# Kernel optimization log

Measured on AMD Instinct MI355X. Metric: run time of the kernel, lower is better.

Reference implementation:

```python
import jax, jax.numpy as jnp
import numpy as np

N_NODES = 50000
N_EDGES = 800000
NODE_DIM = 64
EDGE_DIM = 32
HIDDEN = 128
OUT_DIM = 32
N_LAYERS = 3
NUM_GRAPHS = 128


def setup_inputs() -> dict:
    key = jax.random.key(0)
    ks = jax.random.split(key, 20)
    s = 0.05
    inp = {
        "x": jax.random.normal(ks[0], (N_NODES, NODE_DIM), dtype=jnp.float32),
        "edge_attr": jax.random.normal(ks[1], (N_EDGES, EDGE_DIM), dtype=jnp.float32),
        "edge_index": jax.random.randint(ks[2], (2, N_EDGES), 0, N_NODES, dtype=jnp.int32),
        "batch": jnp.sort(jax.random.randint(ks[3], (N_NODES,), 0, NUM_GRAPHS, dtype=jnp.int32)),
        # per-interaction params, stacked on leading layer axis
        "W_dense": jax.random.normal(ks[4], (N_LAYERS, NODE_DIM, NODE_DIM)) * s,
        "filt_W1": jax.random.normal(ks[5], (N_LAYERS, EDGE_DIM, HIDDEN)) * s,
        "filt_b1": jnp.zeros((N_LAYERS, HIDDEN)),
        "filt_W2": jax.random.normal(ks[6], (N_LAYERS, HIDDEN, NODE_DIM)) * s,
        "filt_b2": jnp.zeros((N_LAYERS, NODE_DIM)),
        "attn_v": jax.random.normal(ks[7], (N_LAYERS, NODE_DIM)) * s,
        "out_W1": jax.random.normal(ks[8], (N_LAYERS, NODE_DIM, HIDDEN)) * s,
        "out_b1": jnp.zeros((N_LAYERS, HIDDEN)),
        "out_W2": jax.random.normal(ks[9], (N_LAYERS, HIDDEN, NODE_DIM)) * s,
        "out_b2": jnp.zeros((N_LAYERS, NODE_DIM)),
        # output network
        "net_W1": jax.random.normal(ks[10], (NODE_DIM, HIDDEN)) * s,
        "net_b1": jnp.zeros((HIDDEN,)),
        "net_W2": jax.random.normal(ks[11], (HIDDEN, OUT_DIM)) * s,
        "net_b2": jnp.zeros((OUT_DIM,)),
    }
    return inp


def _mlp2(x, W1, b1, W2, b2):
    # 2-layer MLP with tanh after first layer (matches MLP(num_layers=2, act='tanh'))
    return jnp.tanh(x @ W1 + b1) @ W2 + b2


def reference(x, edge_attr, W_dense, filt_W1, filt_b1, filt_W2, filt_b2,
              attn_v, out_W1, out_b1, out_W2, out_b2,
              net_W1, net_b1, net_W2, net_b2, edge_index, batch):
    n_nodes = x.shape[0]
    src, tgt = edge_index[0], edge_index[1]
    h = x
    for i in range(N_LAYERS):
        hd = h @ W_dense[i]                                   # initial_dense (no bias)
        edge_w = _mlp2(edge_attr, filt_W1[i], filt_b1[i], filt_W2[i], filt_b2[i])  # [E, D]
        messages = hd[src] * edge_w                           # [E, D]
        # per-target segment softmax over attention scores
        scores = messages @ attn_v[i]                         # [E]
        seg_max = jax.ops.segment_max(scores, tgt, num_segments=n_nodes)
        exp_s = jnp.exp(scores - seg_max[tgt])
        denom = jax.ops.segment_sum(exp_s, tgt, num_segments=n_nodes)
        attn_w = exp_s / denom[tgt]                           # [E]
        messages = messages * attn_w[:, None]
        agg = jax.ops.segment_sum(messages, tgt, num_segments=n_nodes)  # [N, D]
        delta = _mlp2(agg, out_W1[i], out_b1[i], out_W2[i], out_b2[i])
        h = h + delta                                         # residual
    # mean pooling per graph
    pooled = jax.ops.segment_sum(h, batch, num_segments=NUM_GRAPHS)
    counts = jnp.bincount(batch, length=NUM_GRAPHS)
    pooled = pooled / jnp.maximum(counts, 1)[:, None].astype(h.dtype)
    out = _mlp2(pooled, net_W1, net_b1, net_W2, net_b2)       # [G, OUT_DIM]
    return out
```

## Files before the change

### kernel.cpp

```cpp
#include <hip/hip_runtime.h>
#include <hip/hip_bf16.h>
#include <math.h>

#define NODE_DIM 64
#define EDGE_DIM 32
#define HIDDEN   128
#define OUT_DIM  32
#define N_LAYERS 3
#define NGRAPH   128

typedef __attribute__((ext_vector_type(8))) short bf16x8;
typedef __attribute__((ext_vector_type(4))) float f32x4;

__device__ __forceinline__ unsigned short f2bf(float f) {
    unsigned u = __float_as_uint(f);
    u = (u + 0x7fffu + ((u >> 16) & 1u)) >> 16;
    return (unsigned short)u;
}
__device__ __forceinline__ float bf2f(unsigned short h) {
    return __uint_as_float((unsigned)h << 16);
}
__device__ __forceinline__ float fast_tanh(float x) {
    float e = __expf(-2.f * x);
    float r = __builtin_amdgcn_rcpf(1.f + e);
    return __builtin_fmaf(2.f, r, -1.f);
}

__global__ __launch_bounds__(256) void coarse_hist_kernel(
    const int* __restrict__ tgt, int* __restrict__ Hc, int E, int C, int NB) {
    __shared__ int lh[512];
    int blk = blockIdx.x, tid = threadIdx.x;
    for (int b = tid; b < C; b += 256) lh[b] = 0;
    __syncthreads();
    int base = blk * 4096;
#pragma unroll
    for (int i = 0; i < 16; ++i) {
        int e = base + i * 256 + tid;
        if (e < E) atomicAdd(&lh[tgt[e] >> 7], 1);
    }
    __syncthreads();
    for (int b = tid; b < C; b += 256) Hc[(size_t)b * NB + blk] = lh[b];
}

__global__ __launch_bounds__(256) void scan1_kernel(const int* __restrict__ c,
                                                    int* __restrict__ o,
                                                    int* __restrict__ bsum, int n) {
    __shared__ int sh[256];
    int b = blockIdx.x, t = threadIdx.x;
    int i = b * 256 + t;
    int v = (i < n) ? c[i] : 0;
    sh[t] = v;
    __syncthreads();
    for (int d = 1; d < 256; d <<= 1) {
        int u = (t >= d) ? sh[t - d] : 0;
        __syncthreads();
        sh[t] += u;
        __syncthreads();
    }
    if (i < n) o[i] = sh[t] - v;
    if (t == 255) bsum[b] = sh[255];
}

__global__ void scan2_kernel(int* __restrict__ bsum, int nb) {
    __shared__ int sh[1024];
    int t = threadIdx.x;
    int v = (t < nb) ? bsum[t] : 0;
    sh[t] = v;
    __syncthreads();
    for (int d = 1; d < 1024; d <<= 1) {
        int u = (t >= d) ? sh[t - d] : 0;
        __syncthreads();
        sh[t] += u;
        __syncthreads();
    }
    if (t < nb) bsum[t] = sh[t] - v;
}

__global__ __launch_bounds__(256) void scan3_kernel(int* __restrict__ o,
                                                    const int* __restrict__ bsum, int n) {
    int i = blockIdx.x * 256 + threadIdx.x;
    if (i < n) o[i] += bsum[blockIdx.x];
}

__global__ __launch_bounds__(256) void coarse_scatter_kernel(
    const int* __restrict__ tgt, const int* __restrict__ Sc,
    int* __restrict__ tgtc, int* __restrict__ ec, int E, int C, int NB) {
    __shared__ int lb[512];
    int blk = blockIdx.x, tid = threadIdx.x;
    for (int b = tid; b < C; b += 256) lb[b] = Sc[(size_t)b * NB + blk];
    __syncthreads();
    int base = blk * 4096;
#pragma unroll
    for (int i = 0; i < 16; ++i) {
        int e = base + i * 256 + tid;
        if (e < E) {
            int t = tgt[e];
            int pos = atomicAdd(&lb[t >> 7], 1);
            tgtc[pos] = t;
            ec[pos] = e;
        }
    }
}

__global__ __launch_bounds__(256) void fine_sort_kernel(
    const int* __restrict__ Sc, const int* __restrict__ tgtc,
    const int* __restrict__ ec, const int* __restrict__ src,
    int* __restrict__ off, int* __restrict__ eidx, int* __restrict__ srcp,
    int E, int N, int C, int NB) {
    __shared__ int fh[128], fs[128], rb[128];
    int b = blockIdx.x, tid = threadIdx.x;
    int cb0 = Sc[(size_t)b * NB];
    int cb1 = (b + 1 < C) ? Sc[(size_t)(b + 1) * NB] : E;
    if (tid < 128) fh[tid] = 0;
    __syncthreads();
    for (int p = cb0 + tid; p < cb1; p += 256) atomicAdd(&fh[tgtc[p] & 127], 1);
    __syncthreads();
    if (tid < 128) fs[tid] = fh[tid];
    __syncthreads();
    for (int d = 1; d < 128; d <<= 1) {
        int v = 0;
        if (tid < 128 && tid >= d) v = fs[tid - d];
        __syncthreads();
        if (tid < 128) fs[tid] += v;
        __syncthreads();
    }
    if (tid < 128) {
        int ex = fs[tid] - fh[tid];
        rb[tid] = ex;
        int node = (b << 7) + tid;
        if (node < N) off[node] = cb0 + ex;
    }
    if (b == C - 1 && tid == 0) off[N] = E;
    __syncthreads();
    for (int p = cb0 + tid; p < cb1; p += 256) {
        int t = tgtc[p];
        int r = atomicAdd(&rb[t & 127], 1);
        int fpos = cb0 + r;
        int e = ec[p];
        eidx[fpos] = e;
        srcp[fpos] = src[e];
    }
}

__global__ void gbound_kernel(const int* __restrict__ batch, int* __restrict__ goff,
                              int N, int G) {
    int i = blockIdx.x * 256 + threadIdx.x;
    if (i >= N) return;
    int b = batch[i];
    if (i == 0) {
        for (int g = 0; g <= b; ++g) goff[g] = 0;
    } else {
        int bp = batch[i - 1];
        for (int g = bp + 1; g <= b; ++g) goff[g] = i;
    }
    if (i == N - 1) {
        for (int g = b + 1; g <= G; ++g) goff[g] = N;
    }
}

__global__ __launch_bounds__(256) void perm_ea_kernel(
    const float* __restrict__ ea, const int* __restrict__ eidx,
    unsigned short* __restrict__ out, int E) {
    int p = blockIdx.x * 256 + threadIdx.x;
    if (p >= E) return;
    int e = eidx[p];
    const float4* r = (const float4*)(ea + (size_t)e * EDGE_DIM);
    union { unsigned short us[EDGE_DIM]; uint4 u4[EDGE_DIM / 8]; } tmp;
#pragma unroll
    for (int q = 0; q < EDGE_DIM / 4; ++q) {
        float4 v = r[q];
        tmp.us[4 * q]     = f2bf(v.x);
        tmp.us[4 * q + 1] = f2bf(v.y);
        tmp.us[4 * q + 2] = f2bf(v.z);
        tmp.us[4 * q + 3] = f2bf(v.w);
    }
    uint4* o = (uint4*)(out + (size_t)p * EDGE_DIM);
#pragma unroll
    for (int k = 0; k < EDGE_DIM / 8; ++k) o[k] = tmp.u4[k];
}

__global__ void swizzle_w_kernel(const float* __restrict__ fW1, const float* __restrict__ fW2,
                                 const float* __restrict__ oW1, const float* __restrict__ oW2,
                                 unsigned short* __restrict__ W1sw, unsigned short* __restrict__ W2sw,
                                 unsigned short* __restrict__ oW1sw, unsigned short* __restrict__ oW2sw) {
    int i = blockIdx.x / 56, r = blockIdx.x % 56;
    int L = threadIdx.x;
    int e = L & 15, q = L >> 4;
    const float* W;
    unsigned short* out;
    int K, M, t;
    if (r < 8)       { W = fW1 + (size_t)i * EDGE_DIM * HIDDEN;  out = W1sw  + (size_t)i * 8 * 512;  K = EDGE_DIM; M = HIDDEN;   t = r; }
    else if (r < 24) { W = fW2 + (size_t)i * HIDDEN * NODE_DIM;  out = W2sw  + (size_t)i * 16 * 512; K = HIDDEN;   M = NODE_DIM; t = r - 8; }
    else if (r < 40) { W = oW1 + (size_t)i * NODE_DIM * HIDDEN;  out = oW1sw + (size_t)i * 16 * 512; K = NODE_DIM; M = HIDDEN;   t = r - 24; }
    else             { W = oW2 + (size_t)i * HIDDEN * NODE_DIM;  out = oW2sw + (size_t)i * 16 * 512; K = HIDDEN;   M = NODE_DIM; t = r - 40; }
    int nc = K >> 5;
    int mt = t / nc, s = t - mt * nc;
    union { unsigned short us[8]; uint4 u4; } pk;
#pragma unroll
    for (int j = 0; j < 8; ++j)
        pk.us[j] = f2bf(W[(size_t)(32 * s + 8 * q + j) * M + 16 * mt + e]);
    *(uint4*)(out + ((size_t)t * 64 + L) * 8) = pk.u4;
}

#define HSTRIDE 136

__global__ __launch_bounds__(256, 4) void edge_mfma_kernel(
    const unsigned short* __restrict__ ea_p, const float* __restrict__ hd,
    const unsigned short* __restrict__ W1sw, const float* __restrict__ b1,
    const unsigned short* __restrict__ W2sw, const float* __restrict__ b2,
    const float* __restrict__ av, const int* __restrict__ srcp,
    unsigned short* __restrict__ msg, float* __restrict__ score, int E) {
    __shared__ unsigned short Hl[4][2][16 * HSTRIDE];
    int wave = threadIdx.x >> 6, lane = threadIdx.x & 63;
    int e = lane & 15, q = lane >> 4;
    int p0 = blockIdx.x * 128 + wave * 32;
    if (p0 >= E) return;
    int pA = p0 + e, pB = p0 + 16 + e;
    int pAc = pA < E ? pA : E - 1;
    int pBc = pB < E ? pB : E - 1;
    bool vA = pA < E, vB = pB < E;

    bf16x8 eafA = *(const bf16x8*)(ea_p + (size_t)pAc * EDGE_DIM + q * 8);
    bf16x8 eafB = *(const bf16x8*)(ea_p + (size_t)pBc * EDGE_DIM + q * 8);
    int sA = srcp[pAc];
    int sB = srcp[pBc];
    unsigned short* hrA = &Hl[wave][0][e * HSTRIDE];
    unsigned short* hrB = &Hl[wave][1][e * HSTRIDE];

#pragma unroll
    for (int t = 0; t < 8; ++t) {
        bf16x8 a = *(const bf16x8*)(W1sw + (t * 64 + lane) * 8);
        f32x4 cA = __builtin_amdgcn_mfma_f32_16x16x32_bf16(a, eafA, (f32x4){0.f, 0.f, 0.f, 0.f}, 0, 0, 0);
        f32x4 cB = __builtin_amdgcn_mfma_f32_16x16x32_bf16(a, eafB, (f32x4){0.f, 0.f, 0.f, 0.f}, 0, 0, 0);
        float4 b = *(const float4*)(b1 + 16 * t + 4 * q);
        {
            unsigned h0 = f2bf(fast_tanh(cA[0] + b.x));
            unsigned h1 = f2bf(fast_tanh(cA[1] + b.y));
            unsigned h2 = f2bf(fast_tanh(cA[2] + b.z));
            unsigned h3 = f2bf(fast_tanh(cA[3] + b.w));
            uint2 pk;
            pk.x = h0 | (h1 << 16);
            pk.y = h2 | (h3 << 16);
            *(uint2*)(hrA + 16 * t + 4 * q) = pk;
        }
        {
            unsigned h0 = f2bf(fast_tanh(cB[0] + b.x));
            unsigned h1 = f2bf(fast_tanh(cB[1] + b.y));
            unsigned h2 = f2bf(fast_tanh(cB[2] + b.z));
            unsigned h3 = f2bf(fast_tanh(cB[3] + b.w));
            uint2 pk;
            pk.x = h0 | (h1 << 16);
            pk.y = h2 | (h3 << 16);
            *(uint2*)(hrB + 16 * t + 4 * q) = pk;
        }
    }

    float scA = 0.f, scB = 0.f;
#pragma unroll
    for (int np = 0; np < 2; ++np) {
        float4 hvA[2], hvB[2];
#pragma unroll
        for (int k = 0; k < 2; ++k) {
            hvA[k] = *(const float4*)(hd + (size_t)sA * NODE_DIM + 16 * (2 * np + k) + 4 * q);
            hvB[k] = *(const float4*)(hd + (size_t)sB * NODE_DIM + 16 * (2 * np + k) + 4 * q);
        }
        f32x4 c2A[2] = {{0.f, 0.f, 0.f, 0.f}, {0.f, 0.f, 0.f, 0.f}};
        f32x4 c2B[2] = {{0.f, 0.f, 0.f, 0.f}, {0.f, 0.f, 0.f, 0.f}};
#pragma unroll
        for (int s = 0; s < 4; ++s) {
            bf16x8 hfA = *(const bf16x8*)(hrA + 32 * s + 8 * q);
            bf16x8 hfB = *(const bf16x8*)(hrB + 32 * s + 8 * q);
            bf16x8 a0 = *(const bf16x8*)(W2sw + (((2 * np + 0) * 4 + s) * 64 + lane) * 8);
            bf16x8 a1 = *(const bf16x8*)(W2sw + (((2 * np + 1) * 4 + s) * 64 + lane) * 8);
            c2A[0] = __builtin_amdgcn_mfma_f32_16x16x32_bf16(a0, hfA, c2A[0], 0, 0, 0);
            c2B[0] = __builtin_amdgcn_mfma_f32_16x16x32_bf16(a0, hfB, c2B[0], 0, 0, 0);
            c2A[1] = __builtin_amdgcn_mfma_f32_16x16x32_bf16(a1, hfA, c2A[1], 0, 0, 0);
            c2B[1] = __builtin_amdgcn_mfma_f32_16x16x32_bf16(a1, hfB, c2B[1], 0, 0, 0);
        }
#pragma unroll
        for (int k = 0; k < 2; ++k) {
            int nt = 2 * np + k;
            float4 bb = *(const float4*)(b2 + 16 * nt + 4 * q);
            float4 vv = *(const float4*)(av + 16 * nt + 4 * q);
            {
                float4 hh = hvA[k];
                float m0 = (c2A[k][0] + bb.x) * hh.x;
                float m1 = (c2A[k][1] + bb.y) * hh.y;
                float m2 = (c2A[k][2] + bb.z) * hh.z;
                float m3 = (c2A[k][3] + bb.w) * hh.w;
                uint2 pk;
                pk.x = (unsigned)f2bf(m0) | ((unsigned)f2bf(m1) << 16);
                pk.y = (unsigned)f2bf(m2) | ((unsigned)f2bf(m3) << 16);
                if (vA) *(uint2*)(msg + (size_t)pA * NODE_DIM + 16 * nt + 4 * q) = pk;
                scA += m0 * vv.x + m1 * vv.y + m2 * vv.z + m3 * vv.w;
            }
            {
                float4 hh = hvB[k];
                float m0 = (c2B[k][0] + bb.x) * hh.x;
                float m1 = (c2B[k][1] + bb.y) * hh.y;
                float m2 = (c2B[k][2] + bb.z) * hh.z;
                float m3 = (c2B[k][3] + bb.w) * hh.w;
                uint2 pk;
                pk.x = (unsigned)f2bf(m0) | ((unsigned)f2bf(m1) << 16);
                pk.y = (unsigned)f2bf(m2) | ((unsigned)f2bf(m3) << 16);
                if (vB) *(uint2*)(msg + (size_t)pB * NODE_DIM + 16 * nt + 4 * q) = pk;
                scB += m0 * vv.x + m1 * vv.y + m2 * vv.z + m3 * vv.w;
            }
        }
    }
    scA += __shfl_xor(scA, 16, 64);
    scA += __shfl_xor(scA, 32, 64);
    scB += __shfl_xor(scB, 16, 64);
    scB += __shfl_xor(scB, 32, 64);
    if (q == 0) {
        if (vA) score[pA] = scA;
        if (vB) score[pB] = scB;
    }
}

__global__ __launch_bounds__(256) void node_mlp_kernel(
    const float* __restrict__ agg,
    const unsigned short* __restrict__ W1sw, const float* __restrict__ b1,
    const unsigned short* __restrict__ W2sw, const float* __restrict__ b2,
    float* __restrict__ h, int N) {
    __shared__ unsigned short Hl[4][16 * HSTRIDE];
    int wave = threadIdx.x >> 6, lane = threadIdx.x & 63;
    int e = lane & 15, q = lane >> 4;
    int n0 = (blockIdx.x * 4 + wave) * 16;
    if (n0 >= N) return;
    int ne = n0 + e;
    int neC = ne < N ? ne : N - 1;
    bool ok = ne < N;

    bf16x8 bfr[2];
#pragma unroll
    for (int s = 0; s < 2; ++s) {
        const float4* ar = (const float4*)(agg + (size_t)neC * NODE_DIM + 32 * s + 8 * q);
        float4 x0 = ar[0], x1 = ar[1];
        union { bf16x8 v; unsigned short us[8]; } u;
        u.us[0] = f2bf(x0.x); u.us[1] = f2bf(x0.y);
        u.us[2] = f2bf(x0.z); u.us[3] = f2bf(x0.w);
        u.us[4] = f2bf(x1.x); u.us[5] = f2bf(x1.y);
        u.us[6] = f2bf(x1.z); u.us[7] = f2bf(x1.w);
        bfr[s] = u.v;
    }

    f32x4 c1[8];
#pragma unroll
    for (int t = 0; t < 8; ++t) {
        bf16x8 a0 = *(const bf16x8*)(W1sw + ((t * 2 + 0) * 64 + lane) * 8);
        bf16x8 a1 = *(const bf16x8*)(W1sw + ((t * 2 + 1) * 64 + lane) * 8);
        c1[t] = __builtin_amdgcn_mfma_f32_16x16x32_bf16(a0, bfr[0], (f32x4){0.f, 0.f, 0.f, 0.f}, 0, 0, 0);
        c1[t] = __builtin_amdgcn_mfma_f32_16x16x32_bf16(a1, bfr[1], c1[t], 0, 0, 0);
    }

    unsigned short* hrow = &Hl[wave][e * HSTRIDE];
#pragma unroll
    for (int t = 0; t < 8; ++t) {
        float4 b = *(const float4*)(b1 + 16 * t + 4 * q);
        unsigned h0 = f2bf(fast_tanh(c1[t][0] + b.x));
        unsigned h1 = f2bf(fast_tanh(c1[t][1] + b.y));
        unsigned h2 = f2bf(fast_tanh(c1[t][2] + b.z));
        unsigned h3 = f2bf(fast_tanh(c1[t][3] + b.w));
        uint2 pk;
        pk.x = h0 | (h1 << 16);
        pk.y = h2 | (h3 << 16);
        *(uint2*)(hrow + 16 * t + 4 * q) = pk;
    }

    f32x4 c2[4] = {{0.f, 0.f, 0.f, 0.f}, {0.f, 0.f, 0.f, 0.f},
                   {0.f, 0.f, 0.f, 0.f}, {0.f, 0.f, 0.f, 0.f}};
#pragma unroll
    for (int s = 0; s < 4; ++s) {
        bf16x8 hf = *(const bf16x8*)(hrow + 32 * s + 8 * q);
#pragma unroll
        for (int nt = 0; nt < 4; ++nt) {
            bf16x8 a = *(const bf16x8*)(W2sw + ((nt * 4 + s) * 64 + lane) * 8);
            c2[nt] = __builtin_amdgcn_mfma_f32_16x16x32_bf16(a, hf, c2[nt], 0, 0, 0);
        }
    }

    if (ok) {
#pragma unroll
        for (int nt = 0; nt < 4; ++nt) {
            float4 bb = *(const float4*)(b2 + 16 * nt + 4 * q);
            float4* hp = (float4*)(h + (size_t)ne * NODE_DIM + 16 * nt + 4 * q);
            float4 hv = *hp;
            hv.x += c2[nt][0] + bb.x;
            hv.y += c2[nt][1] + bb.y;
            hv.z += c2[nt][2] + bb.z;
            hv.w += c2[nt][3] + bb.w;
            *hp = hv;
        }
    }
}

template <int K, int M, bool ACT, bool RESID>
__global__ __launch_bounds__(256) void dense_kernel(
    const float* __restrict__ X, const float* __restrict__ W,
    const float* __restrict__ bias, float* __restrict__ Y, int rows) {
    int tid = blockIdx.x * 256 + threadIdx.x;
    int row = tid / M;
    int d = tid - row * M;
    if (row >= rows) return;
    if (M >= 64) row = __builtin_amdgcn_readfirstlane(row);
    const float* __restrict__ x = X + (size_t)row * K;
    float acc = bias ? bias[d] : 0.f;
#pragma unroll
    for (int k = 0; k < K; ++k) acc += x[k] * W[k * M + d];
    if (ACT) acc = fast_tanh(acc);
    if (RESID) acc += Y[(size_t)row * M + d];
    Y[(size_t)row * M + d] = acc;
}

__global__ __launch_bounds__(256) void agg_kernel(
    const unsigned short* __restrict__ msg, const float* __restrict__ score,
    const int* __restrict__ off, float* __restrict__ agg, int n) {
    int tid = blockIdx.x * 256 + threadIdx.x;
    int wid = tid >> 6;
    int lane = threadIdx.x & 63;
    if (wid >= n) return;
    wid = __builtin_amdgcn_readfirstlane(wid);
    int o0 = off[wid], o1 = off[wid + 1];
    int g = lane >> 3, s = lane & 7;
    if (o1 <= o0) {
        if (g == 0) {
            float4 z = {0.f, 0.f, 0.f, 0.f};
            float4* dst = (float4*)(agg + (size_t)wid * NODE_DIM + s * 8);
            dst[0] = z; dst[1] = z;
        }
        return;
    }
    float den = 0.f;
    float acc[8] = {0.f, 0.f, 0.f, 0.f, 0.f, 0.f, 0.f, 0.f};
    for (int p = o0; p < o1; p += 8) {
        int pe = p + g;
        int pc = (pe < o1) ? pe : (o1 - 1);
        float w = (pe < o1) ? __expf(fminf(score[pc], 60.f)) : 0.f;
        den += w;
        union { bf16x8 v; unsigned short us[8]; } eu;
        eu.v = *(const bf16x8*)(msg + (size_t)pc * NODE_DIM + s * 8);
        acc[0] += w * bf2f(eu.us[0]);
        acc[1] += w * bf2f(eu.us[1]);
        acc[2] += w * bf2f(eu.us[2]);
        acc[3] += w * bf2f(eu.us[3]);
        acc[4] += w * bf2f(eu.us[4]);
        acc[5] += w * bf2f(eu.us[5]);
        acc[6] += w * bf2f(eu.us[6]);
        acc[7] += w * bf2f(eu.us[7]);
    }
#pragma unroll
    for (int j = 0; j < 8; ++j) {
        acc[j] += __shfl_xor(acc[j], 8, 64);
        acc[j] += __shfl_xor(acc[j], 16, 64);
        acc[j] += __shfl_xor(acc[j], 32, 64);
    }
    den += __shfl_xor(den, 8, 64);
    den += __shfl_xor(den, 16, 64);
    den += __shfl_xor(den, 32, 64);
    if (g == 0) {
        float inv = __builtin_amdgcn_rcpf(den);
        inv = inv * (2.f - den * inv);
        float4 r0 = {acc[0] * inv, acc[1] * inv, acc[2] * inv, acc[3] * inv};
        float4 r1 = {acc[4] * inv, acc[5] * inv, acc[6] * inv, acc[7] * inv};
        float4* dst = (float4*)(agg + (size_t)wid * NODE_DIM + s * 8);
        dst[0] = r0; dst[1] = r1;
    }
}

__global__ __launch_bounds__(256) void pool_kernel(const float* __restrict__ h,
                                                   const int* __restrict__ goff,
                                                   float* __restrict__ pooled) {
    __shared__ float sh[4][NODE_DIM];
    int g = blockIdx.x;
    int w = threadIdx.x >> 6, d = threadIdx.x & 63;
    int o0 = goff[g], o1 = goff[g + 1];
    float acc = 0.f;
    for (int n = o0 + w; n < o1; n += 4) acc += h[(size_t)n * NODE_DIM + d];
    sh[w][d] = acc;
    __syncthreads();
    if (w == 0) {
        float sum = sh[0][d] + sh[1][d] + sh[2][d] + sh[3][d];
        int c = o1 - o0;
        if (c < 1) c = 1;
        pooled[g * NODE_DIM + d] = sum / (float)c;
    }
}

extern "C" void kernel_launch(void* const* d_in, const int* in_sizes, int n_in,
                              void* d_out, int out_size, void* d_ws, size_t ws_size,
                              hipStream_t stream) {
    const float* x         = (const float*)d_in[0];
    const float* edge_attr = (const float*)d_in[1];
    const int*   ei        = (const int*)d_in[2];
    const int*   batch     = (const int*)d_in[3];
    const float* Wd        = (const float*)d_in[4];
    const float* fW1       = (const float*)d_in[5];
    const float* fb1       = (const float*)d_in[6];
    const float* fW2       = (const float*)d_in[7];
    const float* fb2       = (const float*)d_in[8];
    const float* av        = (const float*)d_in[9];
    const float* oW1       = (const float*)d_in[10];
    const float* ob1       = (const float*)d_in[11];
    const float* oW2       = (const float*)d_in[12];
    const float* ob2       = (const float*)d_in[13];
    const float* nW1       = (const float*)d_in[14];
    const float* nb1       = (const float*)d_in[15];
    const float* nW2       = (const float*)d_in[16];
    const float* nb2       = (const float*)d_in[17];
    float* out = (float*)d_out;

    const int N = in_sizes[0] / NODE_DIM;
    const int E = in_sizes[2] / 2;
    const int G = NGRAPH;
    const int NB = (E + 4095) / 4096;
    const int C  = (N + 127) >> 7;
    const int SN = C * NB;
    const int SB = (SN + 255) / 256;

    char* base = (char*)d_ws;
    size_t pos = 0;
    auto alloc = [&](size_t bytes) -> void* {
        pos = (pos + 255) & ~(size_t)255;
        void* r = base + pos;
        pos += bytes;
        return r;
    };
    int* Hc   = (int*)alloc((size_t)SN * 4);
    int* Sc   = (int*)alloc(((size_t)SN + 1) * 4);
    int* bsum = (int*)alloc((size_t)1024 * 4);
    int* tgtc = (int*)alloc((size_t)E * 4);
    int* ec   = (int*)alloc((size_t)E * 4);
    int* off  = (int*)alloc((size_t)(N + 1) * 4);
    int* goff = (int*)alloc((size_t)(G + 1) * 4);
    int* eidx = (int*)alloc((size_t)E * 4);
    int* srcp = (int*)alloc((size_t)E * 4);
    float* score = (float*)alloc((size_t)E * 4);
    float* hd    = (float*)alloc((size_t)N * NODE_DIM * 4);
    float* h     = (float*)alloc((size_t)N * NODE_DIM * 4);
    float* agg   = (float*)alloc((size_t)N * NODE_DIM * 4);
    float* pooled = (float*)alloc((size_t)G * NODE_DIM * 4);
    float* t2     = (float*)alloc((size_t)G * HIDDEN * 4);
    unsigned short* ea_p  = (unsigned short*)alloc((size_t)E * EDGE_DIM * 2);
    unsigned short* msg   = (unsigned short*)alloc((size_t)E * NODE_DIM * 2);
    unsigned short* W1sw  = (unsigned short*)alloc((size_t)N_LAYERS * 8 * 512 * 2);
    unsigned short* W2sw  = (unsigned short*)alloc((size_t)N_LAYERS * 16 * 512 * 2);
    unsigned short* oW1sw = (unsigned short*)alloc((size_t)N_LAYERS * 16 * 512 * 2);
    unsigned short* oW2sw = (unsigned short*)alloc((size_t)N_LAYERS * 16 * 512 * 2);
    (void)ws_size;

    const int* src = ei;
    const int* tgt = ei + E;

    coarse_hist_kernel<<<NB, 256, 0, stream>>>(tgt, Hc, E, C, NB);
    scan1_kernel<<<SB, 256, 0, stream>>>(Hc, Sc, bsum, SN);
    scan2_kernel<<<1, 1024, 0, stream>>>(bsum, SB);
    scan3_kernel<<<SB, 256, 0, stream>>>(Sc, bsum, SN);
    coarse_scatter_kernel<<<NB, 256, 0, stream>>>(tgt, Sc, tgtc, ec, E, C, NB);
    fine_sort_kernel<<<C, 256, 0, stream>>>(Sc, tgtc, ec, src, off, eidx, srcp, E, N, C, NB);
    gbound_kernel<<<(N + 255) / 256, 256, 0, stream>>>(batch, goff, N, G);
    perm_ea_kernel<<<(E + 255) / 256, 256, 0, stream>>>(edge_attr, eidx, ea_p, E);
    swizzle_w_kernel<<<N_LAYERS * 56, 64, 0, stream>>>(fW1, fW2, oW1, oW2, W1sw, W2sw, oW1sw, oW2sw);
    hipMemcpyAsync(h, x, (size_t)N * NODE_DIM * 4, hipMemcpyDeviceToDevice, stream);

    const int node_tiles = (N + 15) / 16;
    for (int i = 0; i < N_LAYERS; ++i) {
        dense_kernel<NODE_DIM, NODE_DIM, false, false>
            <<<(N * NODE_DIM + 255) / 256, 256, 0, stream>>>(
                h, Wd + (size_t)i * NODE_DIM * NODE_DIM, nullptr, hd, N);
        edge_mfma_kernel<<<(E + 127) / 128, 256, 0, stream>>>(
            ea_p, hd,
            W1sw + (size_t)i * 8 * 512, fb1 + (size_t)i * HIDDEN,
            W2sw + (size_t)i * 16 * 512, fb2 + (size_t)i * NODE_DIM,
            av + (size_t)i * NODE_DIM, srcp, msg, score, E);
        agg_kernel<<<(N + 3) / 4, 256, 0, stream>>>(msg, score, off, agg, N);
        node_mlp_kernel<<<(node_tiles + 3) / 4, 256, 0, stream>>>(
            agg,
            oW1sw + (size_t)i * 16 * 512, ob1 + (size_t)i * HIDDEN,
            oW2sw + (size_t)i * 16 * 512, ob2 + (size_t)i * NODE_DIM,
            h, N);
    }

    pool_kernel<<<G, 256, 0, stream>>>(h, goff, pooled);
    dense_kernel<NODE_DIM, HIDDEN, true, false>
        <<<(G * HIDDEN + 255) / 256, 256, 0, stream>>>(pooled, nW1, nb1, t2, G);
    dense_kernel<HIDDEN, OUT_DIM, false, false>
        <<<(G * OUT_DIM + 255) / 256, 256, 0, stream>>>(t2, nW2, nb2, out, G);
}
```

Measured before the change: 717.5 us.

## Fuse segment-softmax aggregation into node MLP kernel and precompute exp scores

Merges the per-node softmax aggregation and the node output MLP into one kernel. Each wave aggregates 16 target nodes into shared memory and then runs the MFMA MLP directly, so the fp32 agg buffer no longer makes a round trip through global memory. The exponentiated score is now computed in the edge kernel rather than in the aggregation loop. bf16 packing uses the hardware-style paired conversion intrinsic. The trade-off is that aggregation now runs one node at a time within a wave, which serialises work per wave and adds a block-wide barrier, so latency hiding may suffer.

```diff
diff --git a/kernel.cpp b/kernel.cpp
--- a/kernel.cpp
+++ b/kernel.cpp
@@ -19,6 +19,10 @@
 }
 __device__ __forceinline__ float bf2f(unsigned short h) {
     return __uint_as_float((unsigned)h << 16);
+}
+__device__ __forceinline__ unsigned pkbf(float lo, float hi) {
+    __hip_bfloat162 t = __float22bfloat162_rn(make_float2(lo, hi));
+    return *reinterpret_cast<unsigned*>(&t);
 }
 __device__ __forceinline__ float fast_tanh(float x) {
     float e = __expf(-2.f * x);
@@ -209,7 +213,7 @@
     const unsigned short* __restrict__ W1sw, const float* __restrict__ b1,
     const unsigned short* __restrict__ W2sw, const float* __restrict__ b2,
     const float* __restrict__ av, const int* __restrict__ srcp,
-    unsigned short* __restrict__ msg, float* __restrict__ score, int E) {
+    unsigned short* __restrict__ msg, float* __restrict__ wexp, int E) {
     __shared__ unsigned short Hl[4][2][16 * HSTRIDE];
     int wave = threadIdx.x >> 6, lane = threadIdx.x & 63;
     int e = lane & 15, q = lane >> 4;
@@ -234,23 +238,15 @@
         f32x4 cB = __builtin_amdgcn_mfma_f32_16x16x32_bf16(a, eafB, (f32x4){0.f, 0.f, 0.f, 0.f}, 0, 0, 0);
         float4 b = *(const float4*)(b1 + 16 * t + 4 * q);
         {
-            unsigned h0 = f2bf(fast_tanh(cA[0] + b.x));
-            unsigned h1 = f2bf(fast_tanh(cA[1] + b.y));
-            unsigned h2 = f2bf(fast_tanh(cA[2] + b.z));
-            unsigned h3 = f2bf(fast_tanh(cA[3] + b.w));
             uint2 pk;
-            pk.x = h0 | (h1 << 16);
-            pk.y = h2 | (h3 << 16);
+            pk.x = pkbf(fast_tanh(cA[0] + b.x), fast_tanh(cA[1] + b.y));
+            pk.y = pkbf(fast_tanh(cA[2] + b.z), fast_tanh(cA[3] + b.w));
             *(uint2*)(hrA + 16 * t + 4 * q) = pk;
         }
         {
-            unsigned h0 = f2bf(fast_tanh(cB[0] + b.x));
-            unsigned h1 = f2bf(fast_tanh(cB[1] + b.y));
-            unsigned h2 = f2bf(fast_tanh(cB[2] + b.z));
-            unsigned h3 = f2bf(fast_tanh(cB[3] + b.w));
             uint2 pk;
-            pk.x = h0 | (h1 << 16);
-            pk.y = h2 | (h3 << 16);
+            pk.x = pkbf(fast_tanh(cB[0] + b.x), fast_tanh(cB[1] + b.y));
+            pk.y = pkbf(fast_tanh(cB[2] + b.z), fast_tanh(cB[3] + b.w));
             *(uint2*)(hrB + 16 * t + 4 * q) = pk;
         }
     }
@@ -289,8 +285,8 @@
                 float m2 = (c2A[k][2] + bb.z) * hh.z;
                 float m3 = (c2A[k][3] + bb.w) * hh.w;
                 uint2 pk;
-                pk.x = (unsigned)f2bf(m0) | ((unsigned)f2bf(m1) << 16);
-                pk.y = (unsigned)f2bf(m2) | ((unsigned)f2bf(m3) << 16);
+                pk.x = pkbf(m0, m1);
+                pk.y = pkbf(m2, m3);
                 if (vA) *(uint2*)(msg + (size_t)pA * NODE_DIM + 16 * nt + 4 * q) = pk;
                 scA += m0 * vv.x + m1 * vv.y + m2 * vv.z + m3 * vv.w;
             }
@@ -301,8 +297,8 @@
                 float m2 = (c2B[k][2] + bb.z) * hh.z;
                 float m3 = (c2B[k][3] + bb.w) * hh.w;
                 uint2 pk;
-                pk.x = (unsigned)f2bf(m0) | ((unsigned)f2bf(m1) << 16);
-                pk.y = (unsigned)f2bf(m2) | ((unsigned)f2bf(m3) << 16);
+                pk.x = pkbf(m0, m1);
+                pk.y = pkbf(m2, m3);
                 if (vB) *(uint2*)(msg + (size_t)pB * NODE_DIM + 16 * nt + 4 * q) = pk;
                 scB += m0 * vv.x + m1 * vv.y + m2 * vv.z + m3 * vv.w;
             }
@@ -313,37 +309,100 @@
     scB += __shfl_xor(scB, 16, 64);
     scB += __shfl_xor(scB, 32, 64);
     if (q == 0) {
-        if (vA) score[pA] = scA;
-        if (vB) score[pB] = scB;
-    }
-}
-
-__global__ __launch_bounds__(256) void node_mlp_kernel(
-    const float* __restrict__ agg,
+        if (vA) wexp[pA] = __expf(fminf(scA, 60.f));
+        if (vB) wexp[pB] = __expf(fminf(scB, 60.f));
+    }
+}
+
+__global__ __launch_bounds__(256) void agg_mlp_kernel(
+    const unsigned short* __restrict__ msg, const float* __restrict__ wexp,
+    const int* __restrict__ off,
     const unsigned short* __restrict__ W1sw, const float* __restrict__ b1,
     const unsigned short* __restrict__ W2sw, const float* __restrict__ b2,
     float* __restrict__ h, int N) {
-    __shared__ unsigned short Hl[4][16 * HSTRIDE];
+    __shared__ float S[4][16 * 68];
     int wave = threadIdx.x >> 6, lane = threadIdx.x & 63;
+    int n0 = blockIdx.x * 64 + wave * 16;
+    bool active = n0 < N;
+    int g = lane >> 3, s = lane & 7;
     int e = lane & 15, q = lane >> 4;
-    int n0 = (blockIdx.x * 4 + wave) * 16;
-    if (n0 >= N) return;
+    float* Sw = &S[wave][0];
+    bf16x8 bfr[2] = {};
+
+    if (active) {
+        int offv = 0;
+        if (lane < 17) {
+            int idx = n0 + lane;
+            offv = off[idx < N ? idx : N];
+        }
+        int imax = (N - n0 < 16) ? (N - n0) : 16;
+        if (g == 0) {
+            float4 z = {0.f, 0.f, 0.f, 0.f};
+            for (int i = imax; i < 16; ++i) {
+                *(float4*)(Sw + i * 68 + s * 8) = z;
+                *(float4*)(Sw + i * 68 + s * 8 + 4) = z;
+            }
+        }
+        for (int i = 0; i < imax; ++i) {
+            int o0 = __shfl(offv, i, 64);
+            int o1 = __shfl(offv, i + 1, 64);
+            float den = 0.f;
+            float acc[8] = {0.f, 0.f, 0.f, 0.f, 0.f, 0.f, 0.f, 0.f};
+            for (int p = o0; p < o1; p += 8) {
+                int pe = p + g;
+                int pc = (pe < o1) ? pe : (o1 - 1);
+                float w = (pe < o1) ? wexp[pc] : 0.f;
+                den += w;
+                union { bf16x8 v; unsigned short us[8]; } eu;
+                eu.v = *(const bf16x8*)(msg + (size_t)pc * NODE_DIM + s * 8);
+                acc[0] += w * bf2f(eu.us[0]);
+                acc[1] += w * bf2f(eu.us[1]);
+                acc[2] += w * bf2f(eu.us[2]);
+                acc[3] += w * bf2f(eu.us[3]);
+                acc[4] += w * bf2f(eu.us[4]);
+                acc[5] += w * bf2f(eu.us[5]);
+                acc[6] += w * bf2f(eu.us[6]);
+                acc[7] += w * bf2f(eu.us[7]);
+            }
+#pragma unroll
+            for (int j = 0; j < 8; ++j) {
+                acc[j] += __shfl_xor(acc[j], 8, 64);
+                acc[j] += __shfl_xor(acc[j], 16, 64);
+                acc[j] += __shfl_xor(acc[j], 32, 64);
+            }
+            den += __shfl_xor(den, 8, 64);
+            den += __shfl_xor(den, 16, 64);
+            den += __shfl_xor(den, 32, 64);
+            if (g == 0) {
+                float inv = 0.f;
+                if (o1 > o0) {
+                    inv = __builtin_amdgcn_rcpf(den);
+                    inv = inv * (2.f - den * inv);
+                }
+                float4 r0 = {acc[0] * inv, acc[1] * inv, acc[2] * inv, acc[3] * inv};
+                float4 r1 = {acc[4] * inv, acc[5] * inv, acc[6] * inv, acc[7] * inv};
+                *(float4*)(Sw + i * 68 + s * 8) = r0;
+                *(float4*)(Sw + i * 68 + s * 8 + 4) = r1;
+            }
+        }
+
+#pragma unroll
+        for (int sp = 0; sp < 2; ++sp) {
+            float4 x0 = *(const float4*)(Sw + e * 68 + 32 * sp + 8 * q);
+            float4 x1 = *(const float4*)(Sw + e * 68 + 32 * sp + 8 * q + 4);
+            union { bf16x8 v; unsigned u[4]; } u;
+            u.u[0] = pkbf(x0.x, x0.y);
+            u.u[1] = pkbf(x0.z, x0.w);
+            u.u[2] = pkbf(x1.x, x1.y);
+            u.u[3] = pkbf(x1.z, x1.w);
+            bfr[sp] = u.v;
+        }
+    }
+    __syncthreads();
+    if (!active) return;
+
     int ne = n0 + e;
-    int neC = ne < N ? ne : N - 1;
     bool ok = ne < N;
-
-    bf16x8 bfr[2];
-#pragma unroll
-    for (int s = 0; s < 2; ++s) {
-        const float4* ar = (const float4*)(agg + (size_t)neC * NODE_DIM + 32 * s + 8 * q);
-        float4 x0 = ar[0], x1 = ar[1];
-        union { bf16x8 v; unsigned short us[8]; } u;
-        u.us[0] = f2bf(x0.x); u.us[1] = f2bf(x0.y);
-        u.us[2] = f2bf(x0.z); u.us[3] = f2bf(x0.w);
-        u.us[4] = f2bf(x1.x); u.us[5] = f2bf(x1.y);
-        u.us[6] = f2bf(x1.z); u.us[7] = f2bf(x1.w);
-        bfr[s] = u.v;
-    }
 
     f32x4 c1[8];
 #pragma unroll
@@ -354,28 +413,24 @@
         c1[t] = __builtin_amdgcn_mfma_f32_16x16x32_bf16(a1, bfr[1], c1[t], 0, 0, 0);
     }
 
-    unsigned short* hrow = &Hl[wave][e * HSTRIDE];
+    unsigned short* hrow = (unsigned short*)Sw + e * HSTRIDE;
 #pragma unroll
     for (int t = 0; t < 8; ++t) {
         float4 b = *(const float4*)(b1 + 16 * t + 4 * q);
-        unsigned h0 = f2bf(fast_tanh(c1[t][0] + b.x));
-        unsigned h1 = f2bf(fast_tanh(c1[t][1] + b.y));
-        unsigned h2 = f2bf(fast_tanh(c1[t][2] + b.z));
-        unsigned h3 = f2bf(fast_tanh(c1[t][3] + b.w));
         uint2 pk;
-        pk.x = h0 | (h1 << 16);
-        pk.y = h2 | (h3 << 16);
+        pk.x = pkbf(fast_tanh(c1[t][0] + b.x), fast_tanh(c1[t][1] + b.y));
+        pk.y = pkbf(fast_tanh(c1[t][2] + b.z), fast_tanh(c1[t][3] + b.w));
         *(uint2*)(hrow + 16 * t + 4 * q) = pk;
     }
 
     f32x4 c2[4] = {{0.f, 0.f, 0.f, 0.f}, {0.f, 0.f, 0.f, 0.f},
                    {0.f, 0.f, 0.f, 0.f}, {0.f, 0.f, 0.f, 0.f}};
 #pragma unroll
-    for (int s = 0; s < 4; ++s) {
-        bf16x8 hf = *(const bf16x8*)(hrow + 32 * s + 8 * q);
+    for (int sp = 0; sp < 4; ++sp) {
+        bf16x8 hf = *(const bf16x8*)(hrow + 32 * sp + 8 * q);
 #pragma unroll
         for (int nt = 0; nt < 4; ++nt) {
-            bf16x8 a = *(const bf16x8*)(W2sw + ((nt * 4 + s) * 64 + lane) * 8);
+            bf16x8 a = *(const bf16x8*)(W2sw + ((nt * 4 + sp) * 64 + lane) * 8);
             c2[nt] = __builtin_amdgcn_mfma_f32_16x16x32_bf16(a, hf, c2[nt], 0, 0, 0);
         }
     }
@@ -411,61 +466,6 @@
     if (ACT) acc = fast_tanh(acc);
     if (RESID) acc += Y[(size_t)row * M + d];
     Y[(size_t)row * M + d] = acc;
-}
-
-__global__ __launch_bounds__(256) void agg_kernel(
-    const unsigned short* __restrict__ msg, const float* __restrict__ score,
-    const int* __restrict__ off, float* __restrict__ agg, int n) {
-    int tid = blockIdx.x * 256 + threadIdx.x;
-    int wid = tid >> 6;
-    int lane = threadIdx.x & 63;
-    if (wid >= n) return;
-    wid = __builtin_amdgcn_readfirstlane(wid);
-    int o0 = off[wid], o1 = off[wid + 1];
-    int g = lane >> 3, s = lane & 7;
-    if (o1 <= o0) {
-        if (g == 0) {
-            float4 z = {0.f, 0.f, 0.f, 0.f};
-            float4* dst = (float4*)(agg + (size_t)wid * NODE_DIM + s * 8);
-            dst[0] = z; dst[1] = z;
-        }
-        return;
-    }
-    float den = 0.f;
-    float acc[8] = {0.f, 0.f, 0.f, 0.f, 0.f, 0.f, 0.f, 0.f};
-    for (int p = o0; p < o1; p += 8) {
-        int pe = p + g;
-        int pc = (pe < o1) ? pe : (o1 - 1);
-        float w = (pe < o1) ? __expf(fminf(score[pc], 60.f)) : 0.f;
-        den += w;
-        union { bf16x8 v; unsigned short us[8]; } eu;
-        eu.v = *(const bf16x8*)(msg + (size_t)pc * NODE_DIM + s * 8);
-        acc[0] += w * bf2f(eu.us[0]);
-        acc[1] += w * bf2f(eu.us[1]);
-        acc[2] += w * bf2f(eu.us[2]);
-        acc[3] += w * bf2f(eu.us[3]);
-        acc[4] += w * bf2f(eu.us[4]);
-        acc[5] += w * bf2f(eu.us[5]);
-        acc[6] += w * bf2f(eu.us[6]);
-        acc[7] += w * bf2f(eu.us[7]);
-    }
-#pragma unroll
-    for (int j = 0; j < 8; ++j) {
-        acc[j] += __shfl_xor(acc[j], 8, 64);
-        acc[j] += __shfl_xor(acc[j], 16, 64);
-        acc[j] += __shfl_xor(acc[j], 32, 64);
-    }
-    den += __shfl_xor(den, 8, 64);
-    den += __shfl_xor(den, 16, 64);
-    den += __shfl_xor(den, 32, 64);
-    if (g == 0) {
-        float inv = __builtin_amdgcn_rcpf(den);
-        inv = inv * (2.f - den * inv);
-        float4 r0 = {acc[0] * inv, acc[1] * inv, acc[2] * inv, acc[3] * inv};
-        float4 r1 = {acc[4] * inv, acc[5] * inv, acc[6] * inv, acc[7] * inv};
-        float4* dst = (float4*)(agg + (size_t)wid * NODE_DIM + s * 8);
-        dst[0] = r0; dst[1] = r1;
-    }
 }
 
 __global__ __launch_bounds__(256) void pool_kernel(const float* __restrict__ h,
@@ -535,10 +535,9 @@
     int* goff = (int*)alloc((size_t)(G + 1) * 4);
     int* eidx = (int*)alloc((size_t)E * 4);
     int* srcp = (int*)alloc((size_t)E * 4);
-    float* score = (float*)alloc((size_t)E * 4);
+    float* wexp = (float*)alloc((size_t)E * 4);
     float* hd    = (float*)alloc((size_t)N * NODE_DIM * 4);
     float* h     = (float*)alloc((size_t)N * NODE_DIM * 4);
-    float* agg   = (float*)alloc((size_t)N * NODE_DIM * 4);
     float* pooled = (float*)alloc((size_t)G * NODE_DIM * 4);
     float* t2     = (float*)alloc((size_t)G * HIDDEN * 4);
     unsigned short* ea_p  = (unsigned short*)alloc((size_t)E * EDGE_DIM * 2);
@@ -563,7 +562,6 @@
     swizzle_w_kernel<<<N_LAYERS * 56, 64, 0, stream>>>(fW1, fW2, oW1, oW2, W1sw, W2sw, oW1sw, oW2sw);
     hipMemcpyAsync(h, x, (size_t)N * NODE_DIM * 4, hipMemcpyDeviceToDevice, stream);
 
-    const int node_tiles = (N + 15) / 16;
     for (int i = 0; i < N_LAYERS; ++i) {
         dense_kernel<NODE_DIM, NODE_DIM, false, false>
             <<<(N * NODE_DIM + 255) / 256, 256, 0, stream>>>(
@@ -572,10 +570,9 @@
             ea_p, hd,
             W1sw + (size_t)i * 8 * 512, fb1 + (size_t)i * HIDDEN,
             W2sw + (size_t)i * 16 * 512, fb2 + (size_t)i * NODE_DIM,
-            av + (size_t)i * NODE_DIM, srcp, msg, score, E);
-        agg_kernel<<<(N + 3) / 4, 256, 0, stream>>>(msg, score, off, agg, N);
-        node_mlp_kernel<<<(node_tiles + 3) / 4, 256, 0, stream>>>(
-            agg,
+            av + (size_t)i * NODE_DIM, srcp, msg, wexp, E);
+        agg_mlp_kernel<<<(N + 63) / 64, 256, 0, stream>>>(
+            msg, wexp, off,
             oW1sw + (size_t)i * 16 * 512, ob1 + (size_t)i * HIDDEN,
             oW2sw + (size_t)i * 16 * 512, ob2 + (size_t)i * NODE_DIM,
             h, N);
```

Result: no change. 717.1 us (-0.1%).
